# Performance work log

Hardware: AMD Instinct MI355X
Metric: run time of the kernel (lower is better)

## Reference

```python
import jax, jax.numpy as jnp
import numpy as np

B, S, E, H = 2, 2048, 2048, 16
D = E // H  # head_dim = 128


def setup_inputs() -> dict:
    key = jax.random.key(0)
    ks = jax.random.split(key, 11)
    scale = 1.0 / np.sqrt(E)
    return {
        "query": jax.random.normal(ks[0], (B, S, E), dtype=jnp.float32),
        "key_in": jax.random.normal(ks[1], (B, S, E), dtype=jnp.float32),
        "value": jax.random.normal(ks[2], (B, S, E), dtype=jnp.float32),
        "Wq": jax.random.normal(ks[3], (E, E), dtype=jnp.float32) * scale,
        "bq": jnp.zeros((E,), dtype=jnp.float32),
        "Wk": jax.random.normal(ks[4], (E, E), dtype=jnp.float32) * scale,
        "bk": jnp.zeros((E,), dtype=jnp.float32),
        "Wv": jax.random.normal(ks[5], (E, E), dtype=jnp.float32) * scale,
        "bv": jnp.zeros((E,), dtype=jnp.float32),
        "Wo": jax.random.normal(ks[6], (E, E), dtype=jnp.float32) * scale,
        "bo": jnp.zeros((E,), dtype=jnp.float32),
    }


def reference(query, key_in, value, Wq, bq, Wk, bk, Wv, bv, Wo, bo):
    # Linear projections then split heads: (B,S,E) -> (B,H,S,D)
    def proj(x, W, b):
        y = x @ W + b
        return y.reshape(B, S, H, D).transpose(0, 2, 1, 3)

    Q = proj(query, Wq, bq)
    K = proj(key_in, Wk, bk)
    V = proj(value, Wv, bv)

    # scores: (B,H,S,S)
    scores = jnp.einsum('bhqd,bhkd->bhqk', Q, K) / jnp.sqrt(jnp.float32(D))
    attn = jax.nn.softmax(scores, axis=-1)
    # attn output: (B,H,S,D) -> (B,S,E)
    out = jnp.einsum('bhqk,bhkd->bhqd', attn, V)
    out = out.transpose(0, 2, 1, 3).reshape(B, S, E)
    return out @ Wo + bo
```

## Files before the change

### kernel.cpp

```cpp
#include <hip/hip_runtime.h>
#include <hip/hip_bf16.h>

typedef __bf16 bf16;
typedef __bf16 bf16x8 __attribute__((ext_vector_type(8)));
typedef float f32x4 __attribute__((ext_vector_type(4)));

constexpr int kE = 2048;
constexpr int kS = 2048;
constexpr int kB = 2;
constexpr int kH = 16;
constexpr int kD = 128;
constexpr int kM = kB * kS;
constexpr float kQScale = 0.12751743f;

#define MFMA_BF16(A, B, C) __builtin_amdgcn_mfma_f32_16x16x32_bf16((A), (B), (C), 0, 0, 0)

__device__ __forceinline__ void async_ld16(const void* gsrc, void* ldst) {
  __builtin_amdgcn_global_load_lds(
      (__attribute__((address_space(1))) void*)(gsrc),
      (__attribute__((address_space(3))) void*)(ldst), 16, 0, 0);
}

__global__ __launch_bounds__(256) void cvt_kernel(
    const float* __restrict__ Xq, const float* __restrict__ Xk,
    const float* __restrict__ Xv, bf16* __restrict__ Y) {
  const int z = blockIdx.y;
  const float* X = (z == 0) ? Xq : (z == 1) ? Xk : Xv;
  bf16* Yz = Y + (size_t)z * kM * kE;
  size_t i = ((size_t)blockIdx.x * 256 + threadIdx.x) * 8;
  float4 v0 = *(const float4*)(X + i);
  float4 v1 = *(const float4*)(X + i + 4);
  bf16x8 hv;
  hv[0] = (bf16)v0.x; hv[1] = (bf16)v0.y; hv[2] = (bf16)v0.z; hv[3] = (bf16)v0.w;
  hv[4] = (bf16)v1.x; hv[5] = (bf16)v1.y; hv[6] = (bf16)v1.z; hv[7] = (bf16)v1.w;
  *(bf16x8*)(Yz + i) = hv;
}

__global__ __launch_bounds__(256) void wt_kernel(
    const float* __restrict__ Wq, const float* __restrict__ Wk,
    const float* __restrict__ Wv, const float* __restrict__ Wo,
    bf16* __restrict__ WT) {
  __shared__ bf16 tile[32][33];
  const int z = blockIdx.z;
  const float* W = (z == 0) ? Wq : (z == 1) ? Wk : (z == 2) ? Wv : Wo;
  const int n0 = blockIdx.x * 32, k0 = blockIdx.y * 32;
  const int tx = threadIdx.x, ty = threadIdx.y;
#pragma unroll
  for (int i = 0; i < 4; ++i) {
    int r = ty + i * 8;
    tile[r][tx] = (bf16)W[(size_t)(k0 + r) * kE + n0 + tx];
  }
  __syncthreads();
#pragma unroll
  for (int i = 0; i < 4; ++i) {
    int r = ty + i * 8;
    WT[(size_t)(z * kE + n0 + r) * kE + k0 + tx] = tile[tx][r];
  }
}

__device__ __forceinline__ void qkv_epilogue(
    const f32x4 acc[4][4], int z, int m0, int n0, int wm, int wn, int ln,
    int qd, const float* bias, bf16* Qb, bf16* Kb, bf16* VTb) {
#pragma unroll
  for (int i = 0; i < 4; ++i) {
    int mbase = m0 + wm * 64 + i * 16 + qd * 4;
#pragma unroll
    for (int j = 0; j < 4; ++j) {
      int n = n0 + wn * 64 + j * 16 + ln;
      float bn = bias[n];
      int h = n >> 7, d = n & 127;
#pragma unroll
      for (int r = 0; r < 4; ++r) {
        int mm = mbase + r;
        int bb = mm >> 11, ss = mm & (kS - 1);
        float v = acc[i][j][r] + bn;
        if (z == 0)
          Qb[((size_t)(bb * kH + h) * kS + ss) * kD + d] = (bf16)(v * kQScale);
        else if (z == 1)
          Kb[((size_t)(bb * kH + h) * kS + ss) * kD + d] = (bf16)v;
        else
          VTb[((size_t)(bb * kH + h) * kD + d) * kS + ss] = (bf16)v;
      }
    }
  }
}

__global__ __launch_bounds__(256) void gemm_qkv_kernel(
    const bf16* __restrict__ Xb, const bf16* __restrict__ WT,
    const float* __restrict__ bq, const float* __restrict__ bk,
    const float* __restrict__ bv, bf16* __restrict__ Qb,
    bf16* __restrict__ Kb, bf16* __restrict__ VTb) {
  __shared__ alignas(16) bf16 As[128 * 64];
  __shared__ alignas(16) bf16 Bs[128 * 64];

  const int z = blockIdx.z;
  const bf16* A = Xb + (size_t)z * kM * kE;
  const float* bias = (z == 0) ? bq : (z == 1) ? bk : bv;
  const bf16* Bt = WT + (size_t)z * kE * kE;

  const int n0 = blockIdx.x * 128;
  const int m0 = blockIdx.y * 128;
  const int t = threadIdx.x;
  const int lane = t & 63;
  const int w = t >> 6;
  const int ln = lane & 15;
  const int qd = lane >> 4;
  const int wm = w >> 1, wn = w & 1;

  const f32x4 fzero = {0.f, 0.f, 0.f, 0.f};
  f32x4 acc[4][4];
#pragma unroll
  for (int i = 0; i < 4; ++i)
#pragma unroll
    for (int j = 0; j < 4; ++j) acc[i][j] = fzero;

  for (int k0 = 0; k0 < kE; k0 += 64) {
    __syncthreads();
#pragma unroll
    for (int i = 0; i < 4; ++i) {
      int c = t + i * 256;
      int row = c >> 3;
      int slot = c & 7;
      int g = slot ^ (row & 7);
      async_ld16(&A[(size_t)(m0 + row) * kE + k0 + g * 8],
                 &As[(size_t)(w * 64 + i * 256) * 8]);
    }
#pragma unroll
    for (int i = 0; i < 4; ++i) {
      int c = t + i * 256;
      int row = c >> 3;
      int slot = c & 7;
      int g = slot ^ (row & 7);
      async_ld16(&Bt[(size_t)(n0 + row) * kE + k0 + g * 8],
                 &Bs[(size_t)(w * 64 + i * 256) * 8]);
    }
    __syncthreads();
#pragma unroll
    for (int ks = 0; ks < 2; ++ks) {
      bf16x8 af[4], bfv[4];
#pragma unroll
      for (int i = 0; i < 4; ++i) {
        int row = wm * 64 + i * 16 + ln;
        int slot = (ks * 4 + qd) ^ (ln & 7);
        af[i] = *(const bf16x8*)&As[row * 64 + slot * 8];
      }
#pragma unroll
      for (int j = 0; j < 4; ++j) {
        int row = wn * 64 + j * 16 + ln;
        int slot = (ks * 4 + qd) ^ (ln & 7);
        bfv[j] = *(const bf16x8*)&Bs[row * 64 + slot * 8];
      }
#pragma unroll
      for (int i = 0; i < 4; ++i)
#pragma unroll
        for (int j = 0; j < 4; ++j)
          acc[i][j] = MFMA_BF16(af[i], bfv[j], acc[i][j]);
    }
  }
  qkv_epilogue(acc, z, m0, n0, wm, wn, ln, qd, bias, Qb, Kb, VTb);
}

__global__ __launch_bounds__(256) void gemm_qkv_f32a_kernel(
    const float* __restrict__ Xq, const float* __restrict__ Xk,
    const float* __restrict__ Xv, const bf16* __restrict__ WT,
    const float* __restrict__ bq, const float* __restrict__ bk,
    const float* __restrict__ bv, bf16* __restrict__ Qb,
    bf16* __restrict__ Kb, bf16* __restrict__ VTb) {
  __shared__ alignas(16) bf16 As[128 * 64];
  __shared__ alignas(16) bf16 Bs[128 * 64];

  const int z = blockIdx.z;
  const float* X = (z == 0) ? Xq : (z == 1) ? Xk : Xv;
  const float* bias = (z == 0) ? bq : (z == 1) ? bk : bv;
  const bf16* Bt = WT + (size_t)z * kE * kE;

  const int n0 = blockIdx.x * 128;
  const int m0 = blockIdx.y * 128;
  const int t = threadIdx.x;
  const int lane = t & 63;
  const int w = t >> 6;
  const int ln = lane & 15;
  const int qd = lane >> 4;
  const int wm = w >> 1, wn = w & 1;

  const f32x4 fzero = {0.f, 0.f, 0.f, 0.f};
  f32x4 acc[4][4];
#pragma unroll
  for (int i = 0; i < 4; ++i)
#pragma unroll
    for (int j = 0; j < 4; ++j) acc[i][j] = fzero;

  for (int k0 = 0; k0 < kE; k0 += 64) {
    __syncthreads();
#pragma unroll
    for (int i = 0; i < 4; ++i) {
      int c = t + i * 256;
      int row = c >> 3;
      int g = c & 7;
      int slot = g ^ (row & 7);
      const float* gp = &X[(size_t)(m0 + row) * kE + k0 + g * 8];
      float4 v0 = *(const float4*)(gp);
      float4 v1 = *(const float4*)(gp + 4);
      bf16x8 hv;
      hv[0] = (bf16)v0.x; hv[1] = (bf16)v0.y; hv[2] = (bf16)v0.z; hv[3] = (bf16)v0.w;
      hv[4] = (bf16)v1.x; hv[5] = (bf16)v1.y; hv[6] = (bf16)v1.z; hv[7] = (bf16)v1.w;
      *(bf16x8*)&As[row * 64 + slot * 8] = hv;
    }
#pragma unroll
    for (int i = 0; i < 4; ++i) {
      int c = t + i * 256;
      int row = c >> 3;
      int slot = c & 7;
      int g = slot ^ (row & 7);
      async_ld16(&Bt[(size_t)(n0 + row) * kE + k0 + g * 8],
                 &Bs[(size_t)(w * 64 + i * 256) * 8]);
    }
    __syncthreads();
#pragma unroll
    for (int ks = 0; ks < 2; ++ks) {
      bf16x8 af[4], bfv[4];
#pragma unroll
      for (int i = 0; i < 4; ++i) {
        int row = wm * 64 + i * 16 + ln;
        int slot = (ks * 4 + qd) ^ (ln & 7);
        af[i] = *(const bf16x8*)&As[row * 64 + slot * 8];
      }
#pragma unroll
      for (int j = 0; j < 4; ++j) {
        int row = wn * 64 + j * 16 + ln;
        int slot = (ks * 4 + qd) ^ (ln & 7);
        bfv[j] = *(const bf16x8*)&Bs[row * 64 + slot * 8];
      }
#pragma unroll
      for (int i = 0; i < 4; ++i)
#pragma unroll
        for (int j = 0; j < 4; ++j)
          acc[i][j] = MFMA_BF16(af[i], bfv[j], acc[i][j]);
    }
  }
  qkv_epilogue(acc, z, m0, n0, wm, wn, ln, qd, bias, Qb, Kb, VTb);
}

__global__ __launch_bounds__(256) void attn_kernel(
    const bf16* __restrict__ Qb, const bf16* __restrict__ Kb,
    const bf16* __restrict__ VTb, bf16* __restrict__ AO) {
  __shared__ alignas(16) bf16 Kt[64 * 128];
  __shared__ alignas(16) bf16 Vt[128 * 64];
  __shared__ alignas(16) bf16 Pl[4][16 * 64];

  const int b = blockIdx.z, h = blockIdx.y;
  const int q0 = blockIdx.x * 64;
  const int t = threadIdx.x, lane = t & 63, w = t >> 6;
  const int ln = lane & 15, qd = lane >> 4;

  const bf16* Qh = Qb + (size_t)(b * kH + h) * kS * kD;
  const bf16* Kh = Kb + (size_t)(b * kH + h) * kS * kD;
  const bf16* Vh = VTb + (size_t)(b * kH + h) * kD * kS;

  bf16x8 qf[4];
  {
    int qr = q0 + w * 16 + ln;
#pragma unroll
    for (int f = 0; f < 4; ++f)
      qf[f] = *(const bf16x8*)&Qh[(size_t)qr * kD + f * 32 + qd * 8];
  }

  const f32x4 fzero = {0.f, 0.f, 0.f, 0.f};
  f32x4 o[8];
#pragma unroll
  for (int dt = 0; dt < 8; ++dt) o[dt] = fzero;
  float lsum[4] = {0.f, 0.f, 0.f, 0.f};

  for (int kc = 0; kc < kS; kc += 64) {
    __syncthreads();
#pragma unroll
    for (int i = 0; i < 4; ++i) {
      int c = t + i * 256;
      int row = c >> 4;
      int slot = c & 15;
      int g = slot ^ (row & 15);
      async_ld16(&Kh[(size_t)(kc + row) * kD + g * 8],
                 &Kt[(size_t)(w * 64 + i * 256) * 8]);
    }
#pragma unroll
    for (int i = 0; i < 4; ++i) {
      int c = t + i * 256;
      int row = c >> 3;
      int slot = c & 7;
      int g = slot ^ (row & 7);
      async_ld16(&Vh[(size_t)row * kS + kc + g * 8],
                 &Vt[(size_t)(w * 64 + i * 256) * 8]);
    }
    __syncthreads();

    f32x4 s[4];
#pragma unroll
    for (int nt = 0; nt < 4; ++nt) s[nt] = fzero;
#pragma unroll
    for (int nt = 0; nt < 4; ++nt) {
      int row = nt * 16 + ln;
#pragma unroll
      for (int f = 0; f < 4; ++f) {
        int slot = (f * 4 + qd) ^ ln;
        bf16x8 kfv = *(const bf16x8*)&Kt[row * 128 + slot * 8];
        s[nt] = MFMA_BF16(qf[f], kfv, s[nt]);
      }
    }

#pragma unroll
    for (int nt = 0; nt < 4; ++nt)
#pragma unroll
      for (int r = 0; r < 4; ++r) {
        float p = __builtin_amdgcn_exp2f(s[nt][r]);
        lsum[r] += p;
        int prow = qd * 4 + r;
        int gchunk = nt * 2 + (ln >> 3);
        int slot = gchunk ^ (prow & 7);
        Pl[w][prow * 64 + slot * 8 + (ln & 7)] = (bf16)p;
      }
    asm volatile("s_waitcnt lgkmcnt(0)" ::: "memory");

    bf16x8 pf[2];
#pragma unroll
    for (int kf = 0; kf < 2; ++kf) {
      int slot = (kf * 4 + qd) ^ (ln & 7);
      pf[kf] = *(const bf16x8*)&Pl[w][ln * 64 + slot * 8];
    }
#pragma unroll
    for (int dt = 0; dt < 8; ++dt) {
      int row = dt * 16 + ln;
#pragma unroll
      for (int kf = 0; kf < 2; ++kf) {
        int slot = (kf * 4 + qd) ^ (ln & 7);
        bf16x8 vv = *(const bf16x8*)&Vt[row * 64 + slot * 8];
        o[dt] = MFMA_BF16(pf[kf], vv, o[dt]);
      }
    }
  }

#pragma unroll
  for (int r = 0; r < 4; ++r) {
    float l = lsum[r];
    l += __shfl_xor(l, 1);
    l += __shfl_xor(l, 2);
    l += __shfl_xor(l, 4);
    l += __shfl_xor(l, 8);
    float inv = 1.f / l;
    int srow = q0 + w * 16 + qd * 4 + r;
    bf16* dst = AO + (size_t)(b * kS + srow) * kE + h * kD;
#pragma unroll
    for (int dt = 0; dt < 8; ++dt)
      dst[dt * 16 + ln] = (bf16)(o[dt][r] * inv);
  }
}

__global__ __launch_bounds__(256) void gemm_out_kernel(
    const bf16* __restrict__ A, const bf16* __restrict__ Bt,
    const float* __restrict__ bias, float* __restrict__ out) {
  __shared__ alignas(16) bf16 As[128 * 64];
  __shared__ alignas(16) bf16 Bs[128 * 64];

  const int n0 = blockIdx.x * 128;
  const int m0 = blockIdx.y * 128;
  const int t = threadIdx.x;
  const int lane = t & 63;
  const int w = t >> 6;
  const int ln = lane & 15;
  const int qd = lane >> 4;
  const int wm = w >> 1, wn = w & 1;

  const f32x4 fzero = {0.f, 0.f, 0.f, 0.f};
  f32x4 acc[4][4];
#pragma unroll
  for (int i = 0; i < 4; ++i)
#pragma unroll
    for (int j = 0; j < 4; ++j) acc[i][j] = fzero;

  for (int k0 = 0; k0 < kE; k0 += 64) {
    __syncthreads();
#pragma unroll
    for (int i = 0; i < 4; ++i) {
      int c = t + i * 256;
      int row = c >> 3;
      int slot = c & 7;
      int g = slot ^ (row & 7);
      async_ld16(&A[(size_t)(m0 + row) * kE + k0 + g * 8],
                 &As[(size_t)(w * 64 + i * 256) * 8]);
    }
#pragma unroll
    for (int i = 0; i < 4; ++i) {
      int c = t + i * 256;
      int row = c >> 3;
      int slot = c & 7;
      int g = slot ^ (row & 7);
      async_ld16(&Bt[(size_t)(n0 + row) * kE + k0 + g * 8],
                 &Bs[(size_t)(w * 64 + i * 256) * 8]);
    }
    __syncthreads();
#pragma unroll
    for (int ks = 0; ks < 2; ++ks) {
      bf16x8 af[4], bfv[4];
#pragma unroll
      for (int i = 0; i < 4; ++i) {
        int row = wm * 64 + i * 16 + ln;
        int slot = (ks * 4 + qd) ^ (ln & 7);
        af[i] = *(const bf16x8*)&As[row * 64 + slot * 8];
      }
#pragma unroll
      for (int j = 0; j < 4; ++j) {
        int row = wn * 64 + j * 16 + ln;
        int slot = (ks * 4 + qd) ^ (ln & 7);
        bfv[j] = *(const bf16x8*)&Bs[row * 64 + slot * 8];
      }
#pragma unroll
      for (int i = 0; i < 4; ++i)
#pragma unroll
        for (int j = 0; j < 4; ++j)
          acc[i][j] = MFMA_BF16(af[i], bfv[j], acc[i][j]);
    }
  }

#pragma unroll
  for (int i = 0; i < 4; ++i) {
    int mbase = m0 + wm * 64 + i * 16 + qd * 4;
#pragma unroll
    for (int j = 0; j < 4; ++j) {
      int n = n0 + wn * 64 + j * 16 + ln;
      float bn = bias[n];
#pragma unroll
      for (int r = 0; r < 4; ++r) {
        int mm = mbase + r;
        out[(size_t)mm * kE + n] = acc[i][j][r] + bn;
      }
    }
  }
}

extern "C" void kernel_launch(void* const* d_in, const int* in_sizes, int n_in,
                              void* d_out, int out_size, void* d_ws,
                              size_t ws_size, hipStream_t stream) {
  const float* query  = (const float*)d_in[0];
  const float* key_in = (const float*)d_in[1];
  const float* value  = (const float*)d_in[2];
  const float* Wq = (const float*)d_in[3];
  const float* bq = (const float*)d_in[4];
  const float* Wk = (const float*)d_in[5];
  const float* bk = (const float*)d_in[6];
  const float* Wv = (const float*)d_in[7];
  const float* bv = (const float*)d_in[8];
  const float* Wo = (const float*)d_in[9];
  const float* bo = (const float*)d_in[10];
  float* out = (float*)d_out;

  const size_t szWT  = (size_t)4 * kE * kE;
  const size_t szAct = (size_t)kM * kE;
  const size_t needBase = (szWT + 4 * szAct) * sizeof(bf16);
  const size_t needFull = needBase + 3 * szAct * sizeof(bf16);
  if (ws_size < needBase) return;

  bf16* WT  = (bf16*)d_ws;
  bf16* Qb  = WT + szWT;
  bf16* Kb  = Qb + szAct;
  bf16* VTb = Kb + szAct;
  bf16* AO  = VTb + szAct;
  bf16* Xb  = AO + szAct;

  wt_kernel<<<dim3(kE / 32, kE / 32, 4), dim3(32, 8), 0, stream>>>(
      Wq, Wk, Wv, Wo, WT);
  if (ws_size >= needFull) {
    cvt_kernel<<<dim3(kM * kE / 8 / 256, 3), 256, 0, stream>>>(
        query, key_in, value, Xb);
    gemm_qkv_kernel<<<dim3(kE / 128, kM / 128, 3), 256, 0, stream>>>(
        Xb, WT, bq, bk, bv, Qb, Kb, VTb);
  } else {
    gemm_qkv_f32a_kernel<<<dim3(kE / 128, kM / 128, 3), 256, 0, stream>>>(
        query, key_in, value, WT, bq, bk, bv, Qb, Kb, VTb);
  }
  attn_kernel<<<dim3(kS / 64, kH, kB), 256, 0, stream>>>(Qb, Kb, VTb, AO);
  gemm_out_kernel<<<dim3(kE / 128, kM / 128), 256, 0, stream>>>(
      AO, WT + (size_t)3 * kE * kE, bo, out);
}
```

Before: 483.2 us.

## Double query rows per attention block and vectorize weight transpose

The attention kernel now gives each wave 32 query rows (two 16-row groups) instead of 16, so a block covers 128 queries. Each K/V tile staged in shared memory is reused across twice as many MFMAs, halving K/V global traffic and synchronisation per query. The cost is roughly double the accumulator registers, which may lower occupancy, and half as many blocks (512). The weight transpose kernel also switches to 64x64 tiles with float4 loads and 16-byte bf16 stores to cut memory transactions.

```diff
diff --git a/kernel.cpp b/kernel.cpp
--- a/kernel.cpp
+++ b/kernel.cpp
@@ -40,21 +40,32 @@
     const float* __restrict__ Wq, const float* __restrict__ Wk,
     const float* __restrict__ Wv, const float* __restrict__ Wo,
     bf16* __restrict__ WT) {
-  __shared__ bf16 tile[32][33];
+  __shared__ bf16 tl[64][72];
   const int z = blockIdx.z;
   const float* W = (z == 0) ? Wq : (z == 1) ? Wk : (z == 2) ? Wv : Wo;
-  const int n0 = blockIdx.x * 32, k0 = blockIdx.y * 32;
-  const int tx = threadIdx.x, ty = threadIdx.y;
-#pragma unroll
-  for (int i = 0; i < 4; ++i) {
-    int r = ty + i * 8;
-    tile[r][tx] = (bf16)W[(size_t)(k0 + r) * kE + n0 + tx];
+  const int n0 = blockIdx.x * 64, k0 = blockIdx.y * 64;
+  const int t = threadIdx.x;
+
+  {
+    const int k = t >> 2, nq = (t & 3) * 16;
+    const float* src = &W[(size_t)(k0 + k) * kE + n0 + nq];
+#pragma unroll
+    for (int u = 0; u < 4; ++u) {
+      float4 v = *(const float4*)(src + u * 4);
+      tl[nq + u * 4 + 0][k] = (bf16)v.x;
+      tl[nq + u * 4 + 1][k] = (bf16)v.y;
+      tl[nq + u * 4 + 2][k] = (bf16)v.z;
+      tl[nq + u * 4 + 3][k] = (bf16)v.w;
+    }
   }
   __syncthreads();
-#pragma unroll
-  for (int i = 0; i < 4; ++i) {
-    int r = ty + i * 8;
-    WT[(size_t)(z * kE + n0 + r) * kE + k0 + tx] = tile[tx][r];
+  {
+    const int n = t >> 2, seg = (t & 3) * 16;
+    bf16x8 a = *(const bf16x8*)&tl[n][seg];
+    bf16x8 b2 = *(const bf16x8*)&tl[n][seg + 8];
+    bf16* dst = &WT[(size_t)(z * kE + n0 + n) * kE + k0 + seg];
+    *(bf16x8*)dst = a;
+    *(bf16x8*)(dst + 8) = b2;
   }
 }
 
@@ -246,10 +257,10 @@
     const bf16* __restrict__ VTb, bf16* __restrict__ AO) {
   __shared__ alignas(16) bf16 Kt[64 * 128];
   __shared__ alignas(16) bf16 Vt[128 * 64];
-  __shared__ alignas(16) bf16 Pl[4][16 * 64];
+  __shared__ alignas(16) bf16 Pl[4][32 * 64];
 
   const int b = blockIdx.z, h = blockIdx.y;
-  const int q0 = blockIdx.x * 64;
+  const int q0 = blockIdx.x * 128;
   const int t = threadIdx.x, lane = t & 63, w = t >> 6;
   const int ln = lane & 15, qd = lane >> 4;
 
@@ -257,19 +268,22 @@
   const bf16* Kh = Kb + (size_t)(b * kH + h) * kS * kD;
   const bf16* Vh = VTb + (size_t)(b * kH + h) * kD * kS;
 
-  bf16x8 qf[4];
-  {
-    int qr = q0 + w * 16 + ln;
+  bf16x8 qf[2][4];
+#pragma unroll
+  for (int rg = 0; rg < 2; ++rg) {
+    int qr = q0 + w * 32 + rg * 16 + ln;
 #pragma unroll
     for (int f = 0; f < 4; ++f)
-      qf[f] = *(const bf16x8*)&Qh[(size_t)qr * kD + f * 32 + qd * 8];
+      qf[rg][f] = *(const bf16x8*)&Qh[(size_t)qr * kD + f * 32 + qd * 8];
   }
 
   const f32x4 fzero = {0.f, 0.f, 0.f, 0.f};
-  f32x4 o[8];
-#pragma unroll
-  for (int dt = 0; dt < 8; ++dt) o[dt] = fzero;
-  float lsum[4] = {0.f, 0.f, 0.f, 0.f};
+  f32x4 o[2][8];
+#pragma unroll
+  for (int rg = 0; rg < 2; ++rg)
+#pragma unroll
+    for (int dt = 0; dt < 8; ++dt) o[rg][dt] = fzero;
+  float lsum[2][4] = {{0.f, 0.f, 0.f, 0.f}, {0.f, 0.f, 0.f, 0.f}};
 
   for (int kc = 0; kc < kS; kc += 64) {
     __syncthreads();
@@ -293,9 +307,11 @@
     }
     __syncthreads();
 
-    f32x4 s[4];
-#pragma unroll
-    for (int nt = 0; nt < 4; ++nt) s[nt] = fzero;
+    f32x4 s[2][4];
+#pragma unroll
+    for (int rg = 0; rg < 2; ++rg)
+#pragma unroll
+      for (int nt = 0; nt < 4; ++nt) s[rg][nt] = fzero;
 #pragma unroll
     for (int nt = 0; nt < 4; ++nt) {
       int row = nt * 16 + ln;
@@ -303,29 +319,35 @@
       for (int f = 0; f < 4; ++f) {
         int slot = (f * 4 + qd) ^ ln;
         bf16x8 kfv = *(const bf16x8*)&Kt[row * 128 + slot * 8];
-        s[nt] = MFMA_BF16(qf[f], kfv, s[nt]);
-      }
-    }
-
-#pragma unroll
-    for (int nt = 0; nt < 4; ++nt)
-#pragma unroll
-      for (int r = 0; r < 4; ++r) {
-        float p = __builtin_amdgcn_exp2f(s[nt][r]);
-        lsum[r] += p;
-        int prow = qd * 4 + r;
-        int gchunk = nt * 2 + (ln >> 3);
-        int slot = gchunk ^ (prow & 7);
-        Pl[w][prow * 64 + slot * 8 + (ln & 7)] = (bf16)p;
-      }
+#pragma unroll
+        for (int rg = 0; rg < 2; ++rg)
+          s[rg][nt] = MFMA_BF16(qf[rg][f], kfv, s[rg][nt]);
+      }
+    }
+
+#pragma unroll
+    for (int rg = 0; rg < 2; ++rg)
+#pragma unroll
+      for (int nt = 0; nt < 4; ++nt)
+#pragma unroll
+        for (int r = 0; r < 4; ++r) {
+          float p = __builtin_amdgcn_exp2f(s[rg][nt][r]);
+          lsum[rg][r] += p;
+          int prow = rg * 16 + qd * 4 + r;
+          int gchunk = nt * 2 + (ln >> 3);
+          int slot = gchunk ^ (prow & 7);
+          Pl[w][prow * 64 + slot * 8 + (ln & 7)] = (bf16)p;
+        }
     asm volatile("s_waitcnt lgkmcnt(0)" ::: "memory");
 
-    bf16x8 pf[2];
-#pragma unroll
-    for (int kf = 0; kf < 2; ++kf) {
-      int slot = (kf * 4 + qd) ^ (ln & 7);
-      pf[kf] = *(const bf16x8*)&Pl[w][ln * 64 + slot * 8];
-    }
+    bf16x8 pf[2][2];
+#pragma unroll
+    for (int rg = 0; rg < 2; ++rg)
+#pragma unroll
+      for (int kf = 0; kf < 2; ++kf) {
+        int slot = (kf * 4 + qd) ^ (ln & 7);
+        pf[rg][kf] = *(const bf16x8*)&Pl[w][(rg * 16 + ln) * 64 + slot * 8];
+      }
 #pragma unroll
     for (int dt = 0; dt < 8; ++dt) {
       int row = dt * 16 + ln;
@@ -333,25 +355,29 @@
       for (int kf = 0; kf < 2; ++kf) {
         int slot = (kf * 4 + qd) ^ (ln & 7);
         bf16x8 vv = *(const bf16x8*)&Vt[row * 64 + slot * 8];
-        o[dt] = MFMA_BF16(pf[kf], vv, o[dt]);
-      }
-    }
-  }
-
-#pragma unroll
-  for (int r = 0; r < 4; ++r) {
-    float l = lsum[r];
-    l += __shfl_xor(l, 1);
-    l += __shfl_xor(l, 2);
-    l += __shfl_xor(l, 4);
-    l += __shfl_xor(l, 8);
-    float inv = 1.f / l;
-    int srow = q0 + w * 16 + qd * 4 + r;
-    bf16* dst = AO + (size_t)(b * kS + srow) * kE + h * kD;
-#pragma unroll
-    for (int dt = 0; dt < 8; ++dt)
-      dst[dt * 16 + ln] = (bf16)(o[dt][r] * inv);
-  }
+#pragma unroll
+        for (int rg = 0; rg < 2; ++rg)
+          o[rg][dt] = MFMA_BF16(pf[rg][kf], vv, o[rg][dt]);
+      }
+    }
+  }
+
+#pragma unroll
+  for (int rg = 0; rg < 2; ++rg)
+#pragma unroll
+    for (int r = 0; r < 4; ++r) {
+      float l = lsum[rg][r];
+      l += __shfl_xor(l, 1);
+      l += __shfl_xor(l, 2);
+      l += __shfl_xor(l, 4);
+      l += __shfl_xor(l, 8);
+      float inv = 1.f / l;
+      int srow = q0 + w * 32 + rg * 16 + qd * 4 + r;
+      bf16* dst = AO + (size_t)(b * kS + srow) * kE + h * kD;
+#pragma unroll
+      for (int dt = 0; dt < 8; ++dt)
+        dst[dt * 16 + ln] = (bf16)(o[rg][dt][r] * inv);
+    }
 }
 
 __global__ __launch_bounds__(256) void gemm_out_kernel(
@@ -465,7 +491,7 @@
   bf16* AO  = VTb + szAct;
   bf16* Xb  = AO + szAct;
 
-  wt_kernel<<<dim3(kE / 32, kE / 32, 4), dim3(32, 8), 0, stream>>>(
+  wt_kernel<<<dim3(kE / 64, kE / 64, 4), 256, 0, stream>>>(
       Wq, Wk, Wv, Wo, WT);
   if (ws_size >= needFull) {
     cvt_kernel<<<dim3(kM * kE / 8 / 256, 3), 256, 0, stream>>>(
@@ -476,7 +502,7 @@
     gemm_qkv_f32a_kernel<<<dim3(kE / 128, kM / 128, 3), 256, 0, stream>>>(
         query, key_in, value, WT, bq, bk, bv, Qb, Kb, VTb);
   }
-  attn_kernel<<<dim3(kS / 64, kH, kB), 256, 0, stream>>>(Qb, Kb, VTb, AO);
+  attn_kernel<<<dim3(kS / 128, kH, kB), 256, 0, stream>>>(Qb, Kb, VTb, AO);
   gemm_out_kernel<<<dim3(kE / 128, kM / 128), 256, 0, stream>>>(
       AO, WT + (size_t)3 * kE * kE, bo, out);
 }
```

Result: slower. 522.5 us (+8.1%).
